# Kernel tuning notes

Measured on AMD Instinct MI355X. Metric: run time of the kernel, lower is better.

## Reference

```python
import jax, jax.numpy as jnp
import numpy as np

EPS = 1e-6
N_HEADS = 16

def setup_inputs() -> dict:
    key = jax.random.key(0)
    ks = jax.random.split(key, 5)
    B, N, D = 64, 512, 1024
    x = jax.random.normal(ks[0], (B, N, D), dtype=jnp.float32)
    s = 0.02
    W_q = jax.random.normal(ks[1], (D, D), dtype=jnp.float32) * s
    W_k = jax.random.normal(ks[2], (D, D), dtype=jnp.float32) * s
    W_v = jax.random.normal(ks[3], (D, D), dtype=jnp.float32) * s
    W_o = jax.random.normal(ks[4], (D, D), dtype=jnp.float32) * s
    z = jnp.zeros((D,), dtype=jnp.float32)
    return {"x": x, "W_q": W_q, "b_q": z, "W_k": W_k, "b_k": z,
            "W_v": W_v, "b_v": z, "W_o": W_o, "b_o": z}

def _heads(t, B, N, H, Dk):
    # [B,N,H*Dk] -> [B,H,N,Dk]
    return t.reshape(B, N, H, Dk).transpose(0, 2, 1, 3)

def reference(x, W_q, b_q, W_k, b_k, W_v, b_v, W_o, b_o):
    B, N, Dm = x.shape
    H = N_HEADS
    Dk = Dm // H
    q = _heads(x @ W_q.T + b_q, B, N, H, Dk)
    k = _heads(x @ W_k.T + b_k, B, N, H, Dk)
    v = _heads(x @ W_v.T + b_v, B, N, H, Dk)
    # position decay LUT: exp(-n/N), applied to ReLU feature maps of q and k
    dec = jnp.exp(-jnp.arange(N, dtype=jnp.float32) / N)[None, None, :, None]
    qf = jax.nn.relu(q) * dec  # [B,H,N,Dk]
    kf = jax.nn.relu(k) * dec
    # global (non-causal) summaries: KV = sum_n k_n v_n^T, Ksum = sum_n k_n
    KV = jnp.einsum('bhnd,bhne->bhde', kf, v)      # [B,H,Dk,Dk]
    Ksum = kf.sum(axis=2)                           # [B,H,Dk]
    denom = jnp.einsum('bhnd,bhd->bhn', qf, Ksum) + EPS
    out = jnp.einsum('bhnd,bhde->bhne', qf, KV) / denom[..., None]
    out = out.transpose(0, 2, 1, 3).reshape(B, N, Dm)
    return out @ W_o.T + b_o
```

## Files before the change

### kernel.cpp

```cpp
#include <hip/hip_runtime.h>
#include <hip/hip_bf16.h>

typedef __attribute__((ext_vector_type(8))) __bf16 bf16x8;
typedef __attribute__((ext_vector_type(4))) __bf16 bf16x4;
typedef __attribute__((ext_vector_type(4))) float f32x4;

#define NBATCH 64
#define NSEQ   512
#define DMODEL 1024
#define NHEAD  16
#define DHEAD  64
#define MROWS  (NBATCH * NSEQ)

static __device__ __forceinline__ void gload_lds16(const void* gp, void* lp) {
  __builtin_amdgcn_global_load_lds(
      (__attribute__((address_space(1))) const void*)gp,
      (__attribute__((address_space(3))) void*)lp,
      16, 0, 0);
}

__global__ void cvt_kernel(const float* __restrict__ in, __bf16* __restrict__ out, int n4) {
  int i = blockIdx.x * blockDim.x + threadIdx.x;
  int stride = gridDim.x * blockDim.x;
  for (; i < n4; i += stride) {
    const float4 v = reinterpret_cast<const float4*>(in)[i];
    bf16x4 o;
    o.x = (__bf16)v.x; o.y = (__bf16)v.y; o.z = (__bf16)v.z; o.w = (__bf16)v.w;
    reinterpret_cast<bf16x4*>(out)[i] = o;
  }
}

template <int MODE>
__global__ void gemm_kernel(const __bf16* __restrict__ A, const __bf16* __restrict__ Bw,
                            const float* __restrict__ bias0, const float* __restrict__ bias1,
                            const float* __restrict__ bias2,
                            __bf16* __restrict__ outq, __bf16* __restrict__ outkT,
                            __bf16* __restrict__ outvT, float* __restrict__ outf) {
  constexpr int K = 1024;
  __shared__ __bf16 As[128 * 32];
  __shared__ __bf16 Bs[128 * 32];
  const int tid = threadIdx.x;
  const int l = tid & 63;
  const int w = tid >> 6;
  const int wr = w >> 1, wc = w & 1;
  const int bm = blockIdx.y, bn = blockIdx.x;
  const int m0 = bm * 128, j0 = bn * 128;

  f32x4 acc[4][4] = {};

  const int fb0 = w * 1024;
  const int fb1 = 4096 + w * 1024;
  const int f0 = fb0 + l * 16, f1 = fb1 + l * 16;
  const size_t ga0 = (size_t)(m0 + (f0 >> 6)) * K + ((f0 & 63) >> 1);
  const size_t ga1 = (size_t)(m0 + (f1 >> 6)) * K + ((f1 & 63) >> 1);
  const size_t gb0 = (size_t)(j0 + (f0 >> 6)) * K + ((f0 & 63) >> 1);
  const size_t gb1 = (size_t)(j0 + (f1 >> 6)) * K + ((f1 & 63) >> 1);

  const int lrow = l & 15, lk = (l >> 4) * 8;

  for (int kk = 0; kk < K; kk += 32) {
    gload_lds16(A + ga0 + kk, (char*)As + fb0);
    gload_lds16(A + ga1 + kk, (char*)As + fb1);
    gload_lds16(Bw + gb0 + kk, (char*)Bs + fb0);
    gload_lds16(Bw + gb1 + kk, (char*)Bs + fb1);
    __syncthreads();
    bf16x8 af[4], bfr[4];
#pragma unroll
    for (int mi = 0; mi < 4; mi++)
      af[mi] = *reinterpret_cast<const bf16x8*>(&As[(wr * 64 + mi * 16 + lrow) * 32 + lk]);
#pragma unroll
    for (int ni = 0; ni < 4; ni++)
      bfr[ni] = *reinterpret_cast<const bf16x8*>(&Bs[(wc * 64 + ni * 16 + lrow) * 32 + lk]);
#pragma unroll
    for (int mi = 0; mi < 4; mi++)
#pragma unroll
      for (int ni = 0; ni < 4; ni++)
        acc[mi][ni] = __builtin_amdgcn_mfma_f32_16x16x32_bf16(af[mi], bfr[ni], acc[mi][ni], 0, 0, 0);
    __syncthreads();
  }

  if constexpr (MODE == 0) {
    const int sel = j0 >> 10;
    const int jb = j0 & 1023;
    const float* bias = (sel == 0) ? bias0 : ((sel == 1) ? bias1 : bias2);
#pragma unroll
    for (int mi = 0; mi < 4; mi++) {
      const int mbase = m0 + wr * 64 + mi * 16 + ((l >> 4) << 2);
#pragma unroll
      for (int ni = 0; ni < 4; ni++) {
        const int j = jb + wc * 64 + ni * 16 + lrow;
        const float bv_ = bias[j];
        if (sel == 0) {
#pragma unroll
          for (int r = 0; r < 4; r++) {
            const int m = mbase + r;
            float val = acc[mi][ni][r] + bv_;
            val = fmaxf(val, 0.f) * __expf(-(float)(m & (NSEQ - 1)) * (1.0f / NSEQ));
            outq[(size_t)m * DMODEL + j] = (__bf16)val;
          }
        } else {
          const int bidx = mbase >> 9;
          const int n0 = mbase & (NSEQ - 1);
          __bf16* dst = (sel == 1) ? outkT : outvT;
          bf16x4 pk;
#pragma unroll
          for (int r = 0; r < 4; r++) {
            float val = acc[mi][ni][r] + bv_;
            if (sel == 1)
              val = fmaxf(val, 0.f) * __expf(-(float)(n0 + r) * (1.0f / NSEQ));
            pk[r] = (__bf16)val;
          }
          *reinterpret_cast<bf16x4*>(
              &dst[((size_t)((bidx * NHEAD + (j >> 6)) * DHEAD + (j & 63))) * NSEQ + n0]) = pk;
        }
      }
    }
  } else {
#pragma unroll
    for (int mi = 0; mi < 4; mi++) {
      const int mbase = m0 + wr * 64 + mi * 16 + ((l >> 4) << 2);
#pragma unroll
      for (int ni = 0; ni < 4; ni++) {
        const int j = j0 + wc * 64 + ni * 16 + lrow;
        const float bo = bias0[j];
#pragma unroll
        for (int r = 0; r < 4; r++)
          outf[(size_t)(mbase + r) * DMODEL + j] = acc[mi][ni][r] + bo;
      }
    }
  }
}

__global__ void attn_kernel(const __bf16* __restrict__ qf, const __bf16* __restrict__ kfT,
                            const __bf16* __restrict__ vT, __bf16* __restrict__ attn) {
  const int bh = blockIdx.x;
  const int b = bh >> 4, h = bh & 15;
  const __bf16* kT = kfT + (size_t)bh * DHEAD * NSEQ;
  const __bf16* vTp = vT + (size_t)bh * DHEAD * NSEQ;
  const __bf16* qp = qf + (size_t)b * NSEQ * DMODEL + h * DHEAD;
  __bf16* op = attn + (size_t)b * NSEQ * DMODEL + h * DHEAD;

  const int tid = threadIdx.x;
  const int l = tid & 63;
  const int w = tid >> 6;
  const int lrow = l & 15, lk = (l >> 4) * 8;

  __shared__ __bf16 KVT[64][88];
  __shared__ float Ksum[64];
  __shared__ float ksum_part[4][64];
  __shared__ float denom[512];

  {
    f32x4 kv[4] = {};
    const int arow = w * 16 + lrow;
    for (int kk = 0; kk < NSEQ; kk += 32) {
      bf16x8 a = *reinterpret_cast<const bf16x8*>(&kT[(size_t)arow * NSEQ + kk + lk]);
#pragma unroll
      for (int ni = 0; ni < 4; ni++) {
        bf16x8 bv = *reinterpret_cast<const bf16x8*>(&vTp[(size_t)(ni * 16 + lrow) * NSEQ + kk + lk]);
        kv[ni] = __builtin_amdgcn_mfma_f32_16x16x32_bf16(a, bv, kv[ni], 0, 0, 0);
      }
    }
    const int d0 = w * 16 + ((l >> 4) << 2);
#pragma unroll
    for (int ni = 0; ni < 4; ni++) {
      const int e = ni * 16 + lrow;
      bf16x4 pk;
#pragma unroll
      for (int r = 0; r < 4; r++) pk[r] = (__bf16)kv[ni][r];
      *reinterpret_cast<bf16x4*>(&KVT[e][d0]) = pk;
    }
  }

  {
    const int d = tid & 63, part = tid >> 6;
    float s = 0.f;
    for (int n = part * 128; n < part * 128 + 128; n += 8) {
      bf16x8 kv8 = *reinterpret_cast<const bf16x8*>(&kT[(size_t)d * NSEQ + n]);
#pragma unroll
      for (int j = 0; j < 8; j++) s += (float)kv8[j];
    }
    ksum_part[part][d] = s;
  }
  __syncthreads();
  if (tid < 64)
    Ksum[tid] = ksum_part[0][tid] + ksum_part[1][tid] + ksum_part[2][tid] + ksum_part[3][tid];
  __syncthreads();

  for (int n = tid; n < NSEQ; n += 256) {
    float s = 0.f;
#pragma unroll
    for (int d = 0; d < DHEAD; d += 8) {
      bf16x8 q8 = *reinterpret_cast<const bf16x8*>(&qp[(size_t)n * DMODEL + d]);
#pragma unroll
      for (int j = 0; j < 8; j++) s += (float)q8[j] * Ksum[d + j];
    }
    denom[n] = s + 1e-6f;
  }
  __syncthreads();

  for (int t = 0; t < 8; t++) {
    const int nrow = t * 64 + w * 16 + lrow;
    bf16x8 a0 = *reinterpret_cast<const bf16x8*>(&qp[(size_t)nrow * DMODEL + lk]);
    bf16x8 a1 = *reinterpret_cast<const bf16x8*>(&qp[(size_t)nrow * DMODEL + 32 + lk]);
    f32x4 o[4] = {};
#pragma unroll
    for (int ni = 0; ni < 4; ni++) {
      bf16x8 b0 = *reinterpret_cast<const bf16x8*>(&KVT[ni * 16 + lrow][lk]);
      bf16x8 b1 = *reinterpret_cast<const bf16x8*>(&KVT[ni * 16 + lrow][32 + lk]);
      o[ni] = __builtin_amdgcn_mfma_f32_16x16x32_bf16(a0, b0, o[ni], 0, 0, 0);
      o[ni] = __builtin_amdgcn_mfma_f32_16x16x32_bf16(a1, b1, o[ni], 0, 0, 0);
    }
    const int n0 = t * 64 + w * 16 + ((l >> 4) << 2);
#pragma unroll
    for (int ni = 0; ni < 4; ni++) {
      const int e = ni * 16 + lrow;
#pragma unroll
      for (int r = 0; r < 4; r++)
        op[(size_t)(n0 + r) * DMODEL + e] = (__bf16)(o[ni][r] / denom[n0 + r]);
    }
  }
}

extern "C" void kernel_launch(void* const* d_in, const int* in_sizes, int n_in,
                              void* d_out, int out_size, void* d_ws, size_t ws_size,
                              hipStream_t stream) {
  (void)in_sizes; (void)n_in; (void)out_size; (void)ws_size;
  const float* x  = (const float*)d_in[0];
  const float* Wq = (const float*)d_in[1];
  const float* bq = (const float*)d_in[2];
  const float* Wk = (const float*)d_in[3];
  const float* bk = (const float*)d_in[4];
  const float* Wv = (const float*)d_in[5];
  const float* bv = (const float*)d_in[6];
  const float* Wo = (const float*)d_in[7];
  const float* bo = (const float*)d_in[8];
  float* out = (float*)d_out;

  char* ws = (char*)d_ws;
  __bf16* xb    = (__bf16*)(ws);
  __bf16* qf    = (__bf16*)(ws + 67108864);
  __bf16* kfT   = (__bf16*)(ws + 134217728);
  __bf16* vT    = (__bf16*)(ws + 201326592);
  __bf16* Wqkvb = (__bf16*)(ws + 268435456);
  __bf16* Wob   = (__bf16*)(ws + 274726912);
  __bf16* attnb = xb;

  cvt_kernel<<<4096, 256, 0, stream>>>(x, xb, (MROWS * DMODEL) / 4);
  cvt_kernel<<<1024, 256, 0, stream>>>(Wq, Wqkvb,                 (DMODEL * DMODEL) / 4);
  cvt_kernel<<<1024, 256, 0, stream>>>(Wk, Wqkvb + DMODEL * DMODEL,     (DMODEL * DMODEL) / 4);
  cvt_kernel<<<1024, 256, 0, stream>>>(Wv, Wqkvb + 2 * DMODEL * DMODEL, (DMODEL * DMODEL) / 4);
  cvt_kernel<<<1024, 256, 0, stream>>>(Wo, Wob, (DMODEL * DMODEL) / 4);

  gemm_kernel<0><<<dim3(24, 256), 256, 0, stream>>>(xb, Wqkvb, bq, bk, bv,
                                                    qf, kfT, vT, nullptr);
  attn_kernel<<<NBATCH * NHEAD, 256, 0, stream>>>(qf, kfT, vT, attnb);
  gemm_kernel<1><<<dim3(8, 256), 256, 0, stream>>>(attnb, Wob, bo, nullptr, nullptr,
                                                   nullptr, nullptr, nullptr, out);
}
```

Measured before the change: 508.4 us.

## Replace 128x128 GEMM with 256x256 double-buffered pipelined GEMM using swizzled LDS

Rewrites both projection GEMMs as 256x256-tile kernels with 8 waves, 128KB of dynamic LDS in two buffers, and a staged global-to-LDS prefetch that overlaps the next tiles' loads with MFMA work. It adds an XOR swizzle on LDS addresses to avoid bank conflicts, s_setprio around MFMA bursts, and a block-ID remap that groups workgroups per XCD for L2 reuse. The goal is to cut the per-iteration syncthreads stalls and the low arithmetic intensity of the old 128x128, K=32 loop. The cost is one workgroup per CU with heavy register and LDS use, and intricate vmcnt and barrier accounting.

After: 451.0 us. 11.3% less time.

```diff
diff --git a/kernel.cpp b/kernel.cpp
--- a/kernel.cpp
+++ b/kernel.cpp
@@ -31,52 +31,122 @@
 }
 
 template <int MODE>
-__global__ void gemm_kernel(const __bf16* __restrict__ A, const __bf16* __restrict__ Bw,
-                            const float* __restrict__ bias0, const float* __restrict__ bias1,
-                            const float* __restrict__ bias2,
-                            __bf16* __restrict__ outq, __bf16* __restrict__ outkT,
-                            __bf16* __restrict__ outvT, float* __restrict__ outf) {
+__global__ __launch_bounds__(512, 1)
+void gemm256_kernel(const __bf16* __restrict__ A, const __bf16* __restrict__ Bw,
+                    const float* __restrict__ bias0, const float* __restrict__ bias1,
+                    const float* __restrict__ bias2,
+                    __bf16* __restrict__ outq, __bf16* __restrict__ outkT,
+                    __bf16* __restrict__ outvT, float* __restrict__ outf) {
+  extern __shared__ char smem[];
   constexpr int K = 1024;
-  __shared__ __bf16 As[128 * 32];
-  __shared__ __bf16 Bs[128 * 32];
+  constexpr int NT = K / 64;
+  constexpr int NBN = (MODE == 0) ? 12 : 4;
+  constexpr int NWG = 128 * NBN;
+  constexpr int CPX = NWG / 8;
+
+  const int raw = blockIdx.x;
+  const int wgid = (raw & 7) * CPX + (raw >> 3);
+  const int bm = wgid / NBN;
+  const int bn = wgid - bm * NBN;
+  const int m0 = bm * 256, j0 = bn * 256;
+
   const int tid = threadIdx.x;
   const int l = tid & 63;
   const int w = tid >> 6;
-  const int wr = w >> 1, wc = w & 1;
-  const int bm = blockIdx.y, bn = blockIdx.x;
-  const int m0 = bm * 128, j0 = bn * 128;
-
-  f32x4 acc[4][4] = {};
-
-  const int fb0 = w * 1024;
-  const int fb1 = 4096 + w * 1024;
-  const int f0 = fb0 + l * 16, f1 = fb1 + l * 16;
-  const size_t ga0 = (size_t)(m0 + (f0 >> 6)) * K + ((f0 & 63) >> 1);
-  const size_t ga1 = (size_t)(m0 + (f1 >> 6)) * K + ((f1 & 63) >> 1);
-  const size_t gb0 = (size_t)(j0 + (f0 >> 6)) * K + ((f0 & 63) >> 1);
-  const size_t gb1 = (size_t)(j0 + (f1 >> 6)) * K + ((f1 & 63) >> 1);
-
-  const int lrow = l & 15, lk = (l >> 4) * 8;
-
-  for (int kk = 0; kk < K; kk += 32) {
-    gload_lds16(A + ga0 + kk, (char*)As + fb0);
-    gload_lds16(A + ga1 + kk, (char*)As + fb1);
-    gload_lds16(Bw + gb0 + kk, (char*)Bs + fb0);
-    gload_lds16(Bw + gb1 + kk, (char*)Bs + fb1);
-    __syncthreads();
-    bf16x8 af[4], bfr[4];
+  const int wm = w >> 2, wn = w & 3;
+  const int lrow = l & 15, g16 = l >> 4;
+
+  f32x4 acc[8][4] = {};
+
+  auto stage = [&](int part, int tileIdx) {
+    const int mat = part >> 1, kh = part & 1;
+    const int buf = tileIdx & 1;
+    char* region = smem + (((buf << 2) | (mat << 1) | kh) << 14);
+    const __bf16* src = mat ? Bw : A;
+    const int rowbase = mat ? j0 : m0;
+    const int kk = tileIdx * 64 + kh * 32;
+#pragma unroll
+    for (int i = 0; i < 2; i++) {
+      const int Q = i * 8192 + tid * 16;
+      const int Ls = Q ^ (((Q >> 7) & 3) << 4);
+      gload_lds16(src + (size_t)(rowbase + (Ls >> 6)) * K + kk + ((Ls & 63) >> 1),
+                  region + Q);
+    }
+  };
+
+  auto ldfrag = [&](int mat, int kh, int buf, int row) -> bf16x8 {
+    const int L = row * 64 + g16 * 16;
+    const int phys = L ^ (((row >> 1) & 3) << 4);
+    return *reinterpret_cast<const bf16x8*>(
+        smem + (((buf << 2) | (mat << 1) | kh) << 14) + phys);
+  };
+
+  stage(0, 0); stage(2, 0); stage(3, 0); stage(1, 0);
+  stage(0, 1); stage(2, 1);
+  asm volatile("s_waitcnt vmcnt(4)" ::: "memory");
+  __builtin_amdgcn_s_barrier();
+
+  const int arow = wm * 128 + lrow;
+  const int brow = wn * 64 + lrow;
+
+  for (int T = 0; T < NT; T++) {
+    const int buf = T & 1;
+    bf16x8 a00[4], bk0[4], a10[4];
+#pragma unroll
+    for (int mi = 0; mi < 4; mi++) a00[mi] = ldfrag(0, 0, buf, arow + mi * 16);
+#pragma unroll
+    for (int ni = 0; ni < 4; ni++) bk0[ni] = ldfrag(1, 0, buf, brow + ni * 16);
+#pragma unroll
+    for (int mi = 0; mi < 4; mi++) a10[mi] = ldfrag(0, 0, buf, arow + 64 + mi * 16);
+    if (T + 1 < NT) stage(3, T + 1);
+    __builtin_amdgcn_s_barrier();
+    __builtin_amdgcn_s_setprio(1);
 #pragma unroll
     for (int mi = 0; mi < 4; mi++)
-      af[mi] = *reinterpret_cast<const bf16x8*>(&As[(wr * 64 + mi * 16 + lrow) * 32 + lk]);
-#pragma unroll
-    for (int ni = 0; ni < 4; ni++)
-      bfr[ni] = *reinterpret_cast<const bf16x8*>(&Bs[(wc * 64 + ni * 16 + lrow) * 32 + lk]);
+#pragma unroll
+      for (int ni = 0; ni < 4; ni++)
+        acc[mi][ni] = __builtin_amdgcn_mfma_f32_16x16x32_bf16(a00[mi], bk0[ni], acc[mi][ni], 0, 0, 0);
+    __builtin_amdgcn_s_setprio(0);
+    __builtin_amdgcn_s_barrier();
+    bf16x8 a01[4], bk1[4], a11[4];
+#pragma unroll
+    for (int mi = 0; mi < 4; mi++) a01[mi] = ldfrag(0, 1, buf, arow + mi * 16);
+#pragma unroll
+    for (int ni = 0; ni < 4; ni++) bk1[ni] = ldfrag(1, 1, buf, brow + ni * 16);
+#pragma unroll
+    for (int mi = 0; mi < 4; mi++) a11[mi] = ldfrag(0, 1, buf, arow + 64 + mi * 16);
+    if (T + 1 < NT) stage(1, T + 1);
+    __builtin_amdgcn_s_barrier();
+    __builtin_amdgcn_s_setprio(1);
 #pragma unroll
     for (int mi = 0; mi < 4; mi++)
 #pragma unroll
       for (int ni = 0; ni < 4; ni++)
-        acc[mi][ni] = __builtin_amdgcn_mfma_f32_16x16x32_bf16(af[mi], bfr[ni], acc[mi][ni], 0, 0, 0);
-    __syncthreads();
+        acc[4 + mi][ni] = __builtin_amdgcn_mfma_f32_16x16x32_bf16(a10[mi], bk0[ni], acc[4 + mi][ni], 0, 0, 0);
+    __builtin_amdgcn_s_setprio(0);
+    __builtin_amdgcn_s_barrier();
+    if (T + 2 < NT) stage(0, T + 2);
+    __builtin_amdgcn_s_barrier();
+    __builtin_amdgcn_s_setprio(1);
+#pragma unroll
+    for (int mi = 0; mi < 4; mi++)
+#pragma unroll
+      for (int ni = 0; ni < 4; ni++)
+        acc[mi][ni] = __builtin_amdgcn_mfma_f32_16x16x32_bf16(a01[mi], bk1[ni], acc[mi][ni], 0, 0, 0);
+    __builtin_amdgcn_s_setprio(0);
+    __builtin_amdgcn_s_barrier();
+    if (T + 2 < NT) stage(2, T + 2);
+    __builtin_amdgcn_s_barrier();
+    __builtin_amdgcn_s_setprio(1);
+#pragma unroll
+    for (int mi = 0; mi < 4; mi++)
+#pragma unroll
+      for (int ni = 0; ni < 4; ni++)
+        acc[4 + mi][ni] = __builtin_amdgcn_mfma_f32_16x16x32_bf16(a11[mi], bk1[ni], acc[4 + mi][ni], 0, 0, 0);
+    __builtin_amdgcn_s_setprio(0);
+    if (T < NT - 2)       asm volatile("s_waitcnt vmcnt(4)" ::: "memory");
+    else if (T == NT - 2) asm volatile("s_waitcnt vmcnt(0)" ::: "memory");
+    __builtin_amdgcn_s_barrier();
   }
 
   if constexpr (MODE == 0) {
@@ -84,11 +154,11 @@
     const int jb = j0 & 1023;
     const float* bias = (sel == 0) ? bias0 : ((sel == 1) ? bias1 : bias2);
 #pragma unroll
-    for (int mi = 0; mi < 4; mi++) {
-      const int mbase = m0 + wr * 64 + mi * 16 + ((l >> 4) << 2);
+    for (int mi = 0; mi < 8; mi++) {
+      const int mbase = m0 + wm * 128 + mi * 16 + g16 * 4;
 #pragma unroll
       for (int ni = 0; ni < 4; ni++) {
-        const int j = jb + wc * 64 + ni * 16 + lrow;
+        const int j = jb + wn * 64 + ni * 16 + lrow;
         const float bv_ = bias[j];
         if (sel == 0) {
 #pragma unroll
@@ -117,11 +187,11 @@
     }
   } else {
 #pragma unroll
-    for (int mi = 0; mi < 4; mi++) {
-      const int mbase = m0 + wr * 64 + mi * 16 + ((l >> 4) << 2);
+    for (int mi = 0; mi < 8; mi++) {
+      const int mbase = m0 + wm * 128 + mi * 16 + g16 * 4;
 #pragma unroll
       for (int ni = 0; ni < 4; ni++) {
-        const int j = j0 + wc * 64 + ni * 16 + lrow;
+        const int j = j0 + wn * 64 + ni * 16 + lrow;
         const float bo = bias0[j];
 #pragma unroll
         for (int r = 0; r < 4; r++)
@@ -252,9 +322,9 @@
   cvt_kernel<<<1024, 256, 0, stream>>>(Wv, Wqkvb + 2 * DMODEL * DMODEL, (DMODEL * DMODEL) / 4);
   cvt_kernel<<<1024, 256, 0, stream>>>(Wo, Wob, (DMODEL * DMODEL) / 4);
 
-  gemm_kernel<0><<<dim3(24, 256), 256, 0, stream>>>(xb, Wqkvb, bq, bk, bv,
-                                                    qf, kfT, vT, nullptr);
+  gemm256_kernel<0><<<1536, 512, 131072, stream>>>(xb, Wqkvb, bq, bk, bv,
+                                                   qf, kfT, vT, nullptr);
   attn_kernel<<<NBATCH * NHEAD, 256, 0, stream>>>(qf, kfT, vT, attnb);
-  gemm_kernel<1><<<dim3(8, 256), 256, 0, stream>>>(attnb, Wob, bo, nullptr, nullptr,
-                                                   nullptr, nullptr, nullptr, out);
-}
+  gemm256_kernel<1><<<512, 512, 131072, stream>>>(attnb, Wob, bo, nullptr, nullptr,
+                                                  nullptr, nullptr, nullptr, out);
+}
```
